# Performance work log

Measured on AMD Instinct MI355X. Metric: run time of the kernel, lower is better.

The kernel has to match this reference:

```python
import jax, jax.numpy as jnp
import numpy as np

N_NODES = 50000
N_EDGES = 800000
D_FEAT = 128
UNITS = 256
K = 3


def setup_inputs() -> dict:
    key = jax.random.key(0)
    k1, k2, k3, k4 = jax.random.split(key, 4)
    x = jax.random.normal(k1, (N_NODES, D_FEAT), dtype=jnp.float32)
    edge_index = jax.random.randint(k2, (2, N_EDGES), 0, N_NODES, dtype=jnp.int32)
    edge_weight = jnp.ones((N_EDGES,), dtype=jnp.float32)
    # glorot-uniform kernel [(K+1)*D, UNITS], zero bias
    fan_in, fan_out = D_FEAT * (K + 1), UNITS
    limit = np.sqrt(6.0 / (fan_in + fan_out)).astype(np.float32)
    kernel = jax.random.uniform(k3, (fan_in, fan_out), minval=-limit, maxval=limit, dtype=jnp.float32)
    bias = jnp.zeros((UNITS,), dtype=jnp.float32)
    return {"x": x, "edge_index": edge_index, "edge_weight": edge_weight,
            "kernel": kernel, "bias": bias}


def reference(x, edge_index, edge_weight, kernel, bias):
    n = x.shape[0]
    row, col = edge_index[0], edge_index[1]
    # symmetric GCN normalization (renorm=False: normalize first, then self-loops w=1)
    deg = jax.ops.segment_sum(edge_weight, row, num_segments=n)
    deg_inv_sqrt = jnp.where(deg > 0, jax.lax.rsqrt(jnp.where(deg > 0, deg, 1.0)), 0.0)
    normed_w = deg_inv_sqrt[row] * edge_weight * deg_inv_sqrt[col]
    loop = jnp.arange(n, dtype=row.dtype)
    row2 = jnp.concatenate([row, loop])
    col2 = jnp.concatenate([col, loop])
    w2 = jnp.concatenate([normed_w, jnp.ones((n,), dtype=normed_w.dtype)])
    # K-hop propagation, collecting each hop
    xs = [x]
    h = x
    for _ in range(K):
        msg = h[col2] * w2[:, None]            # [E+N, D] gather + scale
        h = jax.ops.segment_sum(msg, row2, num_segments=n)  # scatter-sum
        xs.append(h)
    hcat = jnp.concatenate(xs, axis=-1)        # [N, (K+1)*D]
    out = hcat @ kernel + bias
    return jax.nn.relu(out)
```

## Files before the change

### kernel.cpp

```cpp
#include <hip/hip_runtime.h>

#define NN 50000
#define NP 50048
#define NE 800000
#define D 128
#define UNITS 256
#define KTOT 512
#define SCAN_NB 50

typedef __attribute__((ext_vector_type(8))) short short8;
typedef __attribute__((ext_vector_type(4))) float floatx4;

__device__ inline unsigned short f2b(float f) {
    unsigned u = __float_as_uint(f);
    return (unsigned short)((u + 0x7fff + ((u >> 16) & 1)) >> 16);
}
__device__ inline float2 bx2f(unsigned v) {
    float2 r;
    r.x = __uint_as_float(v << 16);
    r.y = __uint_as_float(v & 0xffff0000u);
    return r;
}

__global__ void count_kernel(const int* __restrict__ row, int* __restrict__ cnt4,
                             int* __restrict__ rank, int E) {
    int e = blockIdx.x * blockDim.x + threadIdx.x;
    if (e < E) {
        int rep = (e >> 6) & 3;
        rank[e] = atomicAdd(&cnt4[rep * NN + row[e]], 1);
    }
}

__global__ __launch_bounds__(256) void scanA_kernel(int* __restrict__ cnt4,
                                                    int* __restrict__ row_ptr,
                                                    int* __restrict__ bsum) {
    __shared__ int s[256];
    int b = blockIdx.x, t = threadIdx.x;
    int base = b * 1024 + t * 4;
    int v[4];
    int sum = 0;
#pragma unroll
    for (int i = 0; i < 4; ++i) {
        int idx = base + i;
        int tot = 0;
        if (idx < NN) {
            int c0 = cnt4[idx];
            int c1 = cnt4[NN + idx];
            int c2 = cnt4[2 * NN + idx];
            int c3 = cnt4[3 * NN + idx];
            cnt4[idx] = 0;
            cnt4[NN + idx] = c0;
            cnt4[2 * NN + idx] = c0 + c1;
            cnt4[3 * NN + idx] = c0 + c1 + c2;
            tot = c0 + c1 + c2 + c3;
        }
        v[i] = tot;
        sum += tot;
    }
    s[t] = sum;
    __syncthreads();
    for (int off = 1; off < 256; off <<= 1) {
        int add = (t >= off) ? s[t - off] : 0;
        __syncthreads();
        s[t] += add;
        __syncthreads();
    }
    int run = s[t] - sum;
#pragma unroll
    for (int i = 0; i < 4; ++i) {
        int idx = base + i;
        if (idx < NN) row_ptr[idx] = run;
        run += v[i];
    }
    if (t == 255) bsum[b] = s[255];
}

__global__ void scanB_kernel(int* __restrict__ bsum, int* __restrict__ row_ptr) {
    if (threadIdx.x == 0 && blockIdx.x == 0) {
        int run = 0;
        for (int i = 0; i < SCAN_NB; ++i) {
            int v = bsum[i];
            bsum[i] = run;
            run += v;
        }
        row_ptr[NN] = run;
    }
}

__global__ __launch_bounds__(256) void scanC_kernel(int* __restrict__ row_ptr,
                                                    const int* __restrict__ bsum) {
    int b = blockIdx.x, t = threadIdx.x;
    int off = bsum[b];
    int base = b * 1024 + t * 4;
#pragma unroll
    for (int i = 0; i < 4; ++i) {
        int idx = base + i;
        if (idx < NN) row_ptr[idx] += off;
    }
}

__global__ void fill_kernel(const int* __restrict__ row, const int* __restrict__ col,
                            const float* __restrict__ w, const int* __restrict__ rank,
                            const int* __restrict__ row_ptr, const int* __restrict__ cnt4,
                            int2* __restrict__ edges, int E) {
    int e = blockIdx.x * blockDim.x + threadIdx.x;
    if (e >= E) return;
    int r = row[e];
    int rep = (e >> 6) & 3;
    int pos = row_ptr[r] + cnt4[rep * NN + r] + rank[e];
    edges[pos] = make_int2(col[e], __float_as_int(w[e]));
}

__global__ void degdis_kernel(const int* __restrict__ row_ptr, const int2* __restrict__ edges,
                              float* __restrict__ dis) {
    int n = blockIdx.x * blockDim.x + threadIdx.x;
    if (n >= NN) return;
    int beg = row_ptr[n], end = row_ptr[n + 1];
    float s = 0.f;
    for (int e = beg; e < end; ++e) s += __int_as_float(edges[e].y);
    dis[n] = s > 0.f ? rsqrtf(s) : 0.f;
}

__global__ void norm_kernel(const int* __restrict__ row_ptr, const float* __restrict__ dis,
                            int2* __restrict__ edges) {
    int n = blockIdx.x * blockDim.x + threadIdx.x;
    if (n >= NN) return;
    int beg = row_ptr[n], end = row_ptr[n + 1];
    float dr = dis[n];
    for (int e = beg; e < end; ++e) {
        int2 E = edges[e];
        float wn = dr * __int_as_float(E.y) * dis[E.x];
        edges[e].y = __float_as_int(wn);
    }
}

__global__ void convx_kernel(const float* __restrict__ x, unsigned* __restrict__ xb) {
    int t = blockIdx.x * blockDim.x + threadIdx.x;
    float4 v = ((const float4*)x)[t];
    uint2 o;
    o.x = (unsigned)f2b(v.x) | ((unsigned)f2b(v.y) << 16);
    o.y = (unsigned)f2b(v.z) | ((unsigned)f2b(v.w) << 16);
    ((uint2*)xb)[t] = o;
}

__global__ __launch_bounds__(256) void transw_kernel(const float* __restrict__ W,
                                                     short* __restrict__ Wt) {
    __shared__ float tile[32][33];
    int kb = blockIdx.x * 32;
    int nb = blockIdx.y * 32;
    int tx = threadIdx.x & 31, ty = threadIdx.x >> 5;
    for (int i = 0; i < 32; i += 8)
        tile[ty + i][tx] = W[(size_t)(kb + ty + i) * UNITS + nb + tx];
    __syncthreads();
    for (int i = 0; i < 32; i += 8)
        Wt[(size_t)(nb + ty + i) * KTOT + kb + tx] = (short)f2b(tile[tx][ty + i]);
}

__global__ __launch_bounds__(256) void gather_kernel(const unsigned* __restrict__ hprev,
                                                     unsigned* __restrict__ hnext,
                                                     const int* __restrict__ row_ptr,
                                                     const int2* __restrict__ edges) {
    int node = blockIdx.x * 4 + (threadIdx.x >> 6);
    int f = threadIdx.x & 63;
    if (node >= NN) return;
    int beg = row_ptr[node];
    int end = row_ptr[node + 1];
    float2 a = bx2f(hprev[(size_t)node * 64 + f]);
    float ax = a.x, ay = a.y;
    int e = beg;
    for (; e + 8 <= end; e += 8) {
        int2 E0 = edges[e + 0], E1 = edges[e + 1], E2 = edges[e + 2], E3 = edges[e + 3];
        int2 E4 = edges[e + 4], E5 = edges[e + 5], E6 = edges[e + 6], E7 = edges[e + 7];
        float2 v0 = bx2f(hprev[(size_t)E0.x * 64 + f]);
        float2 v1 = bx2f(hprev[(size_t)E1.x * 64 + f]);
        float2 v2 = bx2f(hprev[(size_t)E2.x * 64 + f]);
        float2 v3 = bx2f(hprev[(size_t)E3.x * 64 + f]);
        float2 v4 = bx2f(hprev[(size_t)E4.x * 64 + f]);
        float2 v5 = bx2f(hprev[(size_t)E5.x * 64 + f]);
        float2 v6 = bx2f(hprev[(size_t)E6.x * 64 + f]);
        float2 v7 = bx2f(hprev[(size_t)E7.x * 64 + f]);
        float w0 = __int_as_float(E0.y), w1 = __int_as_float(E1.y);
        float w2 = __int_as_float(E2.y), w3 = __int_as_float(E3.y);
        float w4 = __int_as_float(E4.y), w5 = __int_as_float(E5.y);
        float w6 = __int_as_float(E6.y), w7 = __int_as_float(E7.y);
        ax = fmaf(w0, v0.x, ax); ay = fmaf(w0, v0.y, ay);
        ax = fmaf(w1, v1.x, ax); ay = fmaf(w1, v1.y, ay);
        ax = fmaf(w2, v2.x, ax); ay = fmaf(w2, v2.y, ay);
        ax = fmaf(w3, v3.x, ax); ay = fmaf(w3, v3.y, ay);
        ax = fmaf(w4, v4.x, ax); ay = fmaf(w4, v4.y, ay);
        ax = fmaf(w5, v5.x, ax); ay = fmaf(w5, v5.y, ay);
        ax = fmaf(w6, v6.x, ax); ay = fmaf(w6, v6.y, ay);
        ax = fmaf(w7, v7.x, ax); ay = fmaf(w7, v7.y, ay);
    }
    for (; e < end; ++e) {
        int2 E = edges[e];
        float w = __int_as_float(E.y);
        float2 v = bx2f(hprev[(size_t)E.x * 64 + f]);
        ax = fmaf(w, v.x, ax);
        ay = fmaf(w, v.y, ay);
    }
    hnext[(size_t)node * 64 + f] = (unsigned)f2b(ax) | ((unsigned)f2b(ay) << 16);
}

#define GLDS(g, l)                                                                      \
    __builtin_amdgcn_global_load_lds((const __attribute__((address_space(1))) void*)(g), \
                                     (__attribute__((address_space(3))) void*)(l), 16, 0, 0)

__global__ __launch_bounds__(256) void gemm_mfma(const short* __restrict__ s0,
                                                 const short* __restrict__ s1,
                                                 const short* __restrict__ s2,
                                                 const short* __restrict__ s3,
                                                 const short* __restrict__ Wt,
                                                 const float* __restrict__ bias,
                                                 float* __restrict__ C) {
    __shared__ short As[128 * 32];
    __shared__ short Bs[128 * 32];
    const int t = threadIdx.x;
    const int m0 = blockIdx.x * 128;
    const int n0 = blockIdx.y * 128;
    const int w = t >> 6;
    const int l = t & 63;
    const int wr = (w >> 1) * 64;
    const int wc = (w & 1) * 64;
    const int lm = l & 15;
    const int k8 = (l >> 4) * 8;

    const short* srcs[4] = {s0, s1, s2, s3};

    floatx4 zero = {0.f, 0.f, 0.f, 0.f};
    floatx4 acc[4][4];
#pragma unroll
    for (int r = 0; r < 4; ++r)
#pragma unroll
        for (int c = 0; c < 4; ++c) acc[r][c] = zero;

    const int sm = t >> 2;
    const int sk = (t & 3) * 8;

    for (int kk = 0; kk < KTOT; kk += 32) {
        const short* Asrc = srcs[kk >> 7] + (kk & 127);
        GLDS(Asrc + (size_t)(m0 + sm) * D + sk, As + w * 512);
        GLDS(Asrc + (size_t)(m0 + 64 + sm) * D + sk, As + 2048 + w * 512);
        const short* Bsrc = Wt + kk;
        GLDS(Bsrc + (size_t)(n0 + sm) * KTOT + sk, Bs + w * 512);
        GLDS(Bsrc + (size_t)(n0 + 64 + sm) * KTOT + sk, Bs + 2048 + w * 512);
        __syncthreads();

        short8 af[4], bfr[4];
#pragma unroll
        for (int r = 0; r < 4; ++r)
            af[r] = *(const short8*)&As[(wr + r * 16 + lm) * 32 + k8];
#pragma unroll
        for (int c = 0; c < 4; ++c)
            bfr[c] = *(const short8*)&Bs[(wc + c * 16 + lm) * 32 + k8];
#pragma unroll
        for (int r = 0; r < 4; ++r)
#pragma unroll
            for (int c = 0; c < 4; ++c)
                acc[r][c] = __builtin_amdgcn_mfma_f32_16x16x32_bf16(af[r], bfr[c], acc[r][c], 0, 0, 0);
        __syncthreads();
    }

    const int q4 = (l >> 4) * 4;
#pragma unroll
    for (int r = 0; r < 4; ++r) {
#pragma unroll
        for (int i = 0; i < 4; ++i) {
            int m = m0 + wr + r * 16 + q4 + i;
            if (m < NN) {
#pragma unroll
                for (int c = 0; c < 4; ++c) {
                    int n = n0 + wc + c * 16 + lm;
                    float v = acc[r][c][i] + bias[n];
                    C[(size_t)m * UNITS + n] = fmaxf(v, 0.f);
                }
            }
        }
    }
}

extern "C" void kernel_launch(void* const* d_in, const int* in_sizes, int n_in,
                              void* d_out, int out_size, void* d_ws, size_t ws_size,
                              hipStream_t stream) {
    const float* x = (const float*)d_in[0];
    const int* ei = (const int*)d_in[1];
    const float* ew_in = (const float*)d_in[2];
    const float* W = (const float*)d_in[3];
    const float* bias = (const float*)d_in[4];
    float* out = (float*)d_out;

    const int* row = ei;
    const int* col = ei + NE;

    float* dis = (float*)d_ws;
    int* cnt4 = (int*)(dis + NN);
    int* rank = cnt4 + 4 * NN;
    int* bsum = rank + NE;
    int* row_ptr = bsum + 64;
    int2* edges = (int2*)(row_ptr + NN + 2);
    unsigned* xb = (unsigned*)(edges + NE);
    unsigned* h1b = xb + (size_t)NP * 64;
    unsigned* h2b = h1b + (size_t)NP * 64;
    unsigned* h3b = h2b + (size_t)NP * 64;
    short* Wt = (short*)(h3b + (size_t)NP * 64);

    hipMemsetAsync(cnt4, 0, 4 * NN * sizeof(int), stream);

    count_kernel<<<(NE + 255) / 256, 256, 0, stream>>>(row, cnt4, rank, NE);
    scanA_kernel<<<SCAN_NB, 256, 0, stream>>>(cnt4, row_ptr, bsum);
    scanB_kernel<<<1, 64, 0, stream>>>(bsum, row_ptr);
    scanC_kernel<<<SCAN_NB, 256, 0, stream>>>(row_ptr, bsum);
    fill_kernel<<<(NE + 255) / 256, 256, 0, stream>>>(row, col, ew_in, rank, row_ptr, cnt4,
                                                      edges, NE);
    degdis_kernel<<<(NN + 255) / 256, 256, 0, stream>>>(row_ptr, edges, dis);
    norm_kernel<<<(NN + 255) / 256, 256, 0, stream>>>(row_ptr, dis, edges);

    convx_kernel<<<(NN * D / 4) / 256, 256, 0, stream>>>(x, xb);
    transw_kernel<<<dim3(KTOT / 32, UNITS / 32), 256, 0, stream>>>(W, Wt);

    int gat_blocks = (NN + 3) / 4;
    gather_kernel<<<gat_blocks, 256, 0, stream>>>(xb, h1b, row_ptr, edges);
    gather_kernel<<<gat_blocks, 256, 0, stream>>>(h1b, h2b, row_ptr, edges);
    gather_kernel<<<gat_blocks, 256, 0, stream>>>(h2b, h3b, row_ptr, edges);

    gemm_mfma<<<dim3(NP / 128, UNITS / 128), 256, 0, stream>>>(
        (const short*)xb, (const short*)h1b, (const short*)h2b, (const short*)h3b,
        Wt, bias, out);
}
```

Baseline: 345.4 us.

## Widen atomic replicas, warp-parallel degree/norm, padded gather, swizzled BK=64 GEMM tiles

The count atomics now spread over eight replica counters instead of four, which cuts contention on popular rows. The degree and normalization kernels switch from one thread per node to one wavefront per node, so each wavefront reads a contiguous edge range and sums it with a shuffle reduction. The gather loop pads its tail with zero-weight self reads so every load stays in the unrolled batch of eight. The GEMM moves to K-tiles of 64 with an XOR-swizzled LDS layout to avoid bank conflicts and halve the number of barriers. It also indexes the four feature buffers as one contiguous array, relying on them being laid out back to back in the workspace.

Result: slower. 363.4 us (+5.2%).

```diff
diff --git a/kernel.cpp b/kernel.cpp
--- a/kernel.cpp
+++ b/kernel.cpp
@@ -7,6 +7,7 @@
 #define UNITS 256
 #define KTOT 512
 #define SCAN_NB 50
+#define NREP 8
 
 typedef __attribute__((ext_vector_type(8))) short short8;
 typedef __attribute__((ext_vector_type(4))) float floatx4;
@@ -22,16 +23,16 @@
     return r;
 }
 
-__global__ void count_kernel(const int* __restrict__ row, int* __restrict__ cnt4,
+__global__ void count_kernel(const int* __restrict__ row, int* __restrict__ cnt8,
                              int* __restrict__ rank, int E) {
     int e = blockIdx.x * blockDim.x + threadIdx.x;
     if (e < E) {
-        int rep = (e >> 6) & 3;
-        rank[e] = atomicAdd(&cnt4[rep * NN + row[e]], 1);
-    }
-}
-
-__global__ __launch_bounds__(256) void scanA_kernel(int* __restrict__ cnt4,
+        int rep = (e >> 6) & (NREP - 1);
+        rank[e] = atomicAdd(&cnt8[rep * NN + row[e]], 1);
+    }
+}
+
+__global__ __launch_bounds__(256) void scanA_kernel(int* __restrict__ cnt8,
                                                     int* __restrict__ row_ptr,
                                                     int* __restrict__ bsum) {
     __shared__ int s[256];
@@ -44,15 +45,16 @@
         int idx = base + i;
         int tot = 0;
         if (idx < NN) {
-            int c0 = cnt4[idx];
-            int c1 = cnt4[NN + idx];
-            int c2 = cnt4[2 * NN + idx];
-            int c3 = cnt4[3 * NN + idx];
-            cnt4[idx] = 0;
-            cnt4[NN + idx] = c0;
-            cnt4[2 * NN + idx] = c0 + c1;
-            cnt4[3 * NN + idx] = c0 + c1 + c2;
-            tot = c0 + c1 + c2 + c3;
+            int c[NREP];
+            int run = 0;
+#pragma unroll
+            for (int r = 0; r < NREP; ++r) c[r] = cnt8[r * NN + idx];
+#pragma unroll
+            for (int r = 0; r < NREP; ++r) {
+                cnt8[r * NN + idx] = run;
+                run += c[r];
+            }
+            tot = run;
         }
         v[i] = tot;
         sum += tot;
@@ -101,36 +103,41 @@
 
 __global__ void fill_kernel(const int* __restrict__ row, const int* __restrict__ col,
                             const float* __restrict__ w, const int* __restrict__ rank,
-                            const int* __restrict__ row_ptr, const int* __restrict__ cnt4,
+                            const int* __restrict__ row_ptr, const int* __restrict__ cnt8,
                             int2* __restrict__ edges, int E) {
     int e = blockIdx.x * blockDim.x + threadIdx.x;
     if (e >= E) return;
     int r = row[e];
-    int rep = (e >> 6) & 3;
-    int pos = row_ptr[r] + cnt4[rep * NN + r] + rank[e];
+    int rep = (e >> 6) & (NREP - 1);
+    int pos = row_ptr[r] + cnt8[rep * NN + r] + rank[e];
     edges[pos] = make_int2(col[e], __float_as_int(w[e]));
 }
 
-__global__ void degdis_kernel(const int* __restrict__ row_ptr, const int2* __restrict__ edges,
-                              float* __restrict__ dis) {
-    int n = blockIdx.x * blockDim.x + threadIdx.x;
-    if (n >= NN) return;
-    int beg = row_ptr[n], end = row_ptr[n + 1];
+__global__ __launch_bounds__(256) void degdis_kernel(const int* __restrict__ row_ptr,
+                                                     const int2* __restrict__ edges,
+                                                     float* __restrict__ dis) {
+    int node = blockIdx.x * 4 + (threadIdx.x >> 6);
+    int l = threadIdx.x & 63;
+    if (node >= NN) return;
+    int beg = row_ptr[node], end = row_ptr[node + 1];
     float s = 0.f;
-    for (int e = beg; e < end; ++e) s += __int_as_float(edges[e].y);
-    dis[n] = s > 0.f ? rsqrtf(s) : 0.f;
-}
-
-__global__ void norm_kernel(const int* __restrict__ row_ptr, const float* __restrict__ dis,
-                            int2* __restrict__ edges) {
-    int n = blockIdx.x * blockDim.x + threadIdx.x;
-    if (n >= NN) return;
-    int beg = row_ptr[n], end = row_ptr[n + 1];
-    float dr = dis[n];
-    for (int e = beg; e < end; ++e) {
+    for (int e = beg + l; e < end; e += 64) s += __int_as_float(edges[e].y);
+#pragma unroll
+    for (int off = 32; off; off >>= 1) s += __shfl_down(s, off);
+    if (l == 0) dis[node] = s > 0.f ? rsqrtf(s) : 0.f;
+}
+
+__global__ __launch_bounds__(256) void norm_kernel(const int* __restrict__ row_ptr,
+                                                   const float* __restrict__ dis,
+                                                   int2* __restrict__ edges) {
+    int node = blockIdx.x * 4 + (threadIdx.x >> 6);
+    int l = threadIdx.x & 63;
+    if (node >= NN) return;
+    int beg = row_ptr[node], end = row_ptr[node + 1];
+    float dr = dis[node];
+    for (int e = beg + l; e < end; e += 64) {
         int2 E = edges[e];
-        float wn = dr * __int_as_float(E.y) * dis[E.x];
-        edges[e].y = __float_as_int(wn);
+        edges[e].y = __float_as_int(dr * __int_as_float(E.y) * dis[E.x]);
     }
 }
 
@@ -167,54 +174,43 @@
     int end = row_ptr[node + 1];
     float2 a = bx2f(hprev[(size_t)node * 64 + f]);
     float ax = a.x, ay = a.y;
-    int e = beg;
-    for (; e + 8 <= end; e += 8) {
-        int2 E0 = edges[e + 0], E1 = edges[e + 1], E2 = edges[e + 2], E3 = edges[e + 3];
-        int2 E4 = edges[e + 4], E5 = edges[e + 5], E6 = edges[e + 6], E7 = edges[e + 7];
-        float2 v0 = bx2f(hprev[(size_t)E0.x * 64 + f]);
-        float2 v1 = bx2f(hprev[(size_t)E1.x * 64 + f]);
-        float2 v2 = bx2f(hprev[(size_t)E2.x * 64 + f]);
-        float2 v3 = bx2f(hprev[(size_t)E3.x * 64 + f]);
-        float2 v4 = bx2f(hprev[(size_t)E4.x * 64 + f]);
-        float2 v5 = bx2f(hprev[(size_t)E5.x * 64 + f]);
-        float2 v6 = bx2f(hprev[(size_t)E6.x * 64 + f]);
-        float2 v7 = bx2f(hprev[(size_t)E7.x * 64 + f]);
-        float w0 = __int_as_float(E0.y), w1 = __int_as_float(E1.y);
-        float w2 = __int_as_float(E2.y), w3 = __int_as_float(E3.y);
-        float w4 = __int_as_float(E4.y), w5 = __int_as_float(E5.y);
-        float w6 = __int_as_float(E6.y), w7 = __int_as_float(E7.y);
-        ax = fmaf(w0, v0.x, ax); ay = fmaf(w0, v0.y, ay);
-        ax = fmaf(w1, v1.x, ax); ay = fmaf(w1, v1.y, ay);
-        ax = fmaf(w2, v2.x, ax); ay = fmaf(w2, v2.y, ay);
-        ax = fmaf(w3, v3.x, ax); ay = fmaf(w3, v3.y, ay);
-        ax = fmaf(w4, v4.x, ax); ay = fmaf(w4, v4.y, ay);
-        ax = fmaf(w5, v5.x, ax); ay = fmaf(w5, v5.y, ay);
-        ax = fmaf(w6, v6.x, ax); ay = fmaf(w6, v6.y, ay);
-        ax = fmaf(w7, v7.x, ax); ay = fmaf(w7, v7.y, ay);
-    }
-    for (; e < end; ++e) {
-        int2 E = edges[e];
-        float w = __int_as_float(E.y);
-        float2 v = bx2f(hprev[(size_t)E.x * 64 + f]);
-        ax = fmaf(w, v.x, ax);
-        ay = fmaf(w, v.y, ay);
+    for (int e = beg; e < end; e += 8) {
+        int cidx[8];
+        float wv[8];
+#pragma unroll
+        for (int i = 0; i < 8; ++i) {
+            if (e + i < end) {
+                int2 E = edges[e + i];
+                cidx[i] = E.x;
+                wv[i] = __int_as_float(E.y);
+            } else {
+                cidx[i] = node;
+                wv[i] = 0.f;
+            }
+        }
+        float2 v[8];
+#pragma unroll
+        for (int i = 0; i < 8; ++i) v[i] = bx2f(hprev[(size_t)cidx[i] * 64 + f]);
+#pragma unroll
+        for (int i = 0; i < 8; ++i) {
+            ax = fmaf(wv[i], v[i].x, ax);
+            ay = fmaf(wv[i], v[i].y, ay);
+        }
     }
     hnext[(size_t)node * 64 + f] = (unsigned)f2b(ax) | ((unsigned)f2b(ay) << 16);
 }
 
+#define BK 64
 #define GLDS(g, l)                                                                      \
     __builtin_amdgcn_global_load_lds((const __attribute__((address_space(1))) void*)(g), \
                                      (__attribute__((address_space(3))) void*)(l), 16, 0, 0)
 
-__global__ __launch_bounds__(256) void gemm_mfma(const short* __restrict__ s0,
-                                                 const short* __restrict__ s1,
-                                                 const short* __restrict__ s2,
-                                                 const short* __restrict__ s3,
+__global__ __launch_bounds__(256) void gemm_mfma(const short* __restrict__ A0,
                                                  const short* __restrict__ Wt,
                                                  const float* __restrict__ bias,
                                                  float* __restrict__ C) {
-    __shared__ short As[128 * 32];
-    __shared__ short Bs[128 * 32];
+    __shared__ short As[128 * BK];
+    __shared__ short Bs[128 * BK];
     const int t = threadIdx.x;
     const int m0 = blockIdx.x * 128;
     const int n0 = blockIdx.y * 128;
@@ -223,9 +219,10 @@
     const int wr = (w >> 1) * 64;
     const int wc = (w & 1) * 64;
     const int lm = l & 15;
-    const int k8 = (l >> 4) * 8;
-
-    const short* srcs[4] = {s0, s1, s2, s3};
+    const int lg = l >> 4;
+
+    const int srow = l >> 3;
+    const int soff = ((l & 7) ^ srow) * 8;
 
     floatx4 zero = {0.f, 0.f, 0.f, 0.f};
     floatx4 acc[4][4];
@@ -234,34 +231,43 @@
 #pragma unroll
         for (int c = 0; c < 4; ++c) acc[r][c] = zero;
 
-    const int sm = t >> 2;
-    const int sk = (t & 3) * 8;
-
-    for (int kk = 0; kk < KTOT; kk += 32) {
-        const short* Asrc = srcs[kk >> 7] + (kk & 127);
-        GLDS(Asrc + (size_t)(m0 + sm) * D + sk, As + w * 512);
-        GLDS(Asrc + (size_t)(m0 + 64 + sm) * D + sk, As + 2048 + w * 512);
+    for (int kk = 0; kk < KTOT; kk += BK) {
+        const short* Asrc = A0 + (size_t)(kk >> 7) * ((size_t)NP * 128) + (kk & 127);
         const short* Bsrc = Wt + kk;
-        GLDS(Bsrc + (size_t)(n0 + sm) * KTOT + sk, Bs + w * 512);
-        GLDS(Bsrc + (size_t)(n0 + 64 + sm) * KTOT + sk, Bs + 2048 + w * 512);
+#pragma unroll
+        for (int i = 0; i < 4; ++i) {
+            int seg = w * 4 + i;
+            int row = seg * 8 + srow;
+            GLDS(Asrc + (size_t)(m0 + row) * D + soff, As + seg * 512);
+            GLDS(Bsrc + (size_t)(n0 + row) * KTOT + soff, Bs + seg * 512);
+        }
         __syncthreads();
-
-        short8 af[4], bfr[4];
-#pragma unroll
-        for (int r = 0; r < 4; ++r)
-            af[r] = *(const short8*)&As[(wr + r * 16 + lm) * 32 + k8];
-#pragma unroll
-        for (int c = 0; c < 4; ++c)
-            bfr[c] = *(const short8*)&Bs[(wc + c * 16 + lm) * 32 + k8];
-#pragma unroll
-        for (int r = 0; r < 4; ++r)
-#pragma unroll
-            for (int c = 0; c < 4; ++c)
-                acc[r][c] = __builtin_amdgcn_mfma_f32_16x16x32_bf16(af[r], bfr[c], acc[r][c], 0, 0, 0);
+#pragma unroll
+        for (int j = 0; j < 2; ++j) {
+            short8 af[4], bfr[4];
+#pragma unroll
+            for (int r = 0; r < 4; ++r) {
+                int row = wr + r * 16 + lm;
+                int ch = (lg + 4 * j) ^ (row & 7);
+                af[r] = *(const short8*)&As[row * BK + ch * 8];
+            }
+#pragma unroll
+            for (int c = 0; c < 4; ++c) {
+                int row = wc + c * 16 + lm;
+                int ch = (lg + 4 * j) ^ (row & 7);
+                bfr[c] = *(const short8*)&Bs[row * BK + ch * 8];
+            }
+#pragma unroll
+            for (int r = 0; r < 4; ++r)
+#pragma unroll
+                for (int c = 0; c < 4; ++c)
+                    acc[r][c] = __builtin_amdgcn_mfma_f32_16x16x32_bf16(af[r], bfr[c],
+                                                                        acc[r][c], 0, 0, 0);
+        }
         __syncthreads();
     }
 
-    const int q4 = (l >> 4) * 4;
+    const int q4 = lg * 4;
 #pragma unroll
     for (int r = 0; r < 4; ++r) {
 #pragma unroll
@@ -293,8 +299,8 @@
     const int* col = ei + NE;
 
     float* dis = (float*)d_ws;
-    int* cnt4 = (int*)(dis + NN);
-    int* rank = cnt4 + 4 * NN;
+    int* cnt8 = (int*)(dis + NN);
+    int* rank = cnt8 + NREP * NN;
     int* bsum = rank + NE;
     int* row_ptr = bsum + 64;
     int2* edges = (int2*)(row_ptr + NN + 2);
@@ -304,16 +310,16 @@
     unsigned* h3b = h2b + (size_t)NP * 64;
     short* Wt = (short*)(h3b + (size_t)NP * 64);
 
-    hipMemsetAsync(cnt4, 0, 4 * NN * sizeof(int), stream);
-
-    count_kernel<<<(NE + 255) / 256, 256, 0, stream>>>(row, cnt4, rank, NE);
-    scanA_kernel<<<SCAN_NB, 256, 0, stream>>>(cnt4, row_ptr, bsum);
+    hipMemsetAsync(cnt8, 0, NREP * NN * sizeof(int), stream);
+
+    count_kernel<<<(NE + 255) / 256, 256, 0, stream>>>(row, cnt8, rank, NE);
+    scanA_kernel<<<SCAN_NB, 256, 0, stream>>>(cnt8, row_ptr, bsum);
     scanB_kernel<<<1, 64, 0, stream>>>(bsum, row_ptr);
     scanC_kernel<<<SCAN_NB, 256, 0, stream>>>(row_ptr, bsum);
-    fill_kernel<<<(NE + 255) / 256, 256, 0, stream>>>(row, col, ew_in, rank, row_ptr, cnt4,
+    fill_kernel<<<(NE + 255) / 256, 256, 0, stream>>>(row, col, ew_in, rank, row_ptr, cnt8,
                                                       edges, NE);
-    degdis_kernel<<<(NN + 255) / 256, 256, 0, stream>>>(row_ptr, edges, dis);
-    norm_kernel<<<(NN + 255) / 256, 256, 0, stream>>>(row_ptr, dis, edges);
+    degdis_kernel<<<(NN + 3) / 4, 256, 0, stream>>>(row_ptr, edges, dis);
+    norm_kernel<<<(NN + 3) / 4, 256, 0, stream>>>(row_ptr, dis, edges);
 
     convx_kernel<<<(NN * D / 4) / 256, 256, 0, stream>>>(x, xb);
     transw_kernel<<<dim3(KTOT / 32, UNITS / 32), 256, 0, stream>>>(W, Wt);
@@ -324,6 +330,5 @@
     gather_kernel<<<gat_blocks, 256, 0, stream>>>(h2b, h3b, row_ptr, edges);
 
     gemm_mfma<<<dim3(NP / 128, UNITS / 128), 256, 0, stream>>>(
-        (const short*)xb, (const short*)h1b, (const short*)h2b, (const short*)h3b,
-        Wt, bias, out);
-}
+        (const short*)xb, Wt, bias, out);
+}
```
